# Performance work log

Hardware: AMD Instinct MI355X
Metric: run time of the kernel (lower is better)

Reference implementation:

```python
import jax, jax.numpy as jnp
import numpy as np

NEG_INF = -1e9

def _build_tables():
    # LC0-style 73-plane encoding per from-square: planes 0..55 queen moves
    # (8 directions x 7 distances), 56..63 knight moves. to_sq[from, plane]
    # is the to-square index; valid marks on-board targets.
    to_sq = np.zeros((64, 64), np.int32)
    valid = np.zeros((64, 64), bool)
    dirs = [(1, 0), (1, 1), (0, 1), (-1, 1), (-1, 0), (-1, -1), (0, -1), (1, -1)]
    knights = [(2, 1), (1, 2), (-1, 2), (-2, 1), (-2, -1), (-1, -2), (1, -2), (2, -1)]
    for sq in range(64):
        r, c = divmod(sq, 8)
        for d, (dr, dc) in enumerate(dirs):
            for dist in range(1, 8):
                p = d * 7 + (dist - 1)
                nr, nc = r + dr * dist, c + dc * dist
                if 0 <= nr < 8 and 0 <= nc < 8:
                    to_sq[sq, p] = nr * 8 + nc
                    valid[sq, p] = True
        for i, (dr, dc) in enumerate(knights):
            nr, nc = r + dr, c + dc
            if 0 <= nr < 8 and 0 <= nc < 8:
                to_sq[sq, 56 + i] = nr * 8 + nc
                valid[sq, 56 + i] = True
    promo_from = (np.arange(64) // 8) == 6  # rank 7 pawns (0-indexed rank 6)
    return to_sq, valid, promo_from

TO_SQ_NP, VALID_NP, PROMO_FROM_NP = _build_tables()
TO_SQ = jnp.asarray(TO_SQ_NP)            # (64, 64) int32
TO_VALID = jnp.asarray(VALID_NP)         # (64, 64) bool
PROMO_FROM = jnp.asarray(PROMO_FROM_NP)  # (64,) bool

EMBED_DIM = 1024
POLICY_DIM = 128
SCALE = POLICY_DIM ** (-0.5)


def setup_inputs() -> dict:
    key = jax.random.key(0)
    ks = jax.random.split(key, 4)
    B = 1024
    std = 1.0 / np.sqrt(EMBED_DIM)
    x = jax.random.normal(ks[0], (B, 64, EMBED_DIM), dtype=jnp.float32)
    Wq = jax.random.normal(ks[1], (EMBED_DIM, POLICY_DIM), dtype=jnp.float32) * std
    Wk = jax.random.normal(ks[2], (EMBED_DIM, POLICY_DIM), dtype=jnp.float32) * std
    Wu = jax.random.normal(ks[3], (EMBED_DIM, 9), dtype=jnp.float32) * std
    bq = jnp.zeros((POLICY_DIM,), jnp.float32)
    bk = jnp.zeros((POLICY_DIM,), jnp.float32)
    bu = jnp.zeros((9,), jnp.float32)
    return {"x": x, "Wq": Wq, "bq": bq, "Wk": Wk, "bk": bk, "Wu": Wu, "bu": bu}


def reference(x, Wq, bq, Wk, bk, Wu, bu):
    b = x.shape[0]
    q = jnp.einsum('bsd,dp->bsp', x, Wq) + bq            # (B, 64, P)
    k = jnp.einsum('bsd,dp->bsp', x, Wk) + bk            # (B, 64, P)
    logits_ft = jnp.einsum('bfp,btp->bft', q, k) * SCALE  # (B, 64, 64)
    # gather to-square logits into plane order per from-square
    idx = jnp.broadcast_to(TO_SQ[None].astype(jnp.int32), (b, 64, 64))
    logits_64 = jnp.take_along_axis(logits_ft, idx, axis=-1)  # (B, 64, 64)
    logits_64 = jnp.where(TO_VALID[None], logits_64, jnp.float32(NEG_INF))
    up = jnp.einsum('bsd,dn->bsn', x, Wu) + bu            # (B, 64, 9)
    up = jnp.where(PROMO_FROM[None, :, None], up, jnp.float32(NEG_INF))
    logits = jnp.concatenate([logits_64, up], axis=-1)    # (B, 64, 73)
    return logits.reshape(b, 64 * 73)
```

## Files before the change

### kernel.cpp

```cpp
#include <hip/hip_runtime.h>

#define NEG_INF (-1e9f)
#define SCALE_F 0.08838834764831845f

typedef __attribute__((ext_vector_type(8))) short short8;
typedef __attribute__((ext_vector_type(4))) float float4v;

__device__ __constant__ int cDR[8] = {1,1,0,-1,-1,-1,0,1};
__device__ __constant__ int cDC[8] = {0,1,1,1,0,-1,-1,-1};
__device__ __constant__ int cKR[8] = {2,1,-1,-2,-2,-1,1,2};
__device__ __constant__ int cKC[8] = {1,2,2,1,-1,-2,-2,-1};

__device__ __forceinline__ ushort f2bf(float f) {
  union { float f; unsigned u; } a; a.f = f;
  unsigned u = a.u;
  return (ushort)((u + 0x7FFFu + ((u >> 16) & 1u)) >> 16);
}

__device__ __forceinline__ void glds16(const void* g, void* l) {
  __builtin_amdgcn_global_load_lds(
      (const __attribute__((address_space(1))) unsigned int*)g,
      (__attribute__((address_space(3))) unsigned int*)l, 16, 0, 0);
}

__device__ __forceinline__ short8 pack8(float4 a, float4 b) {
  union { short8 v; unsigned u[4]; } o;
  o.u[0] = (__float_as_uint(a.y) & 0xFFFF0000u) | (__float_as_uint(a.x) >> 16);
  o.u[1] = (__float_as_uint(a.w) & 0xFFFF0000u) | (__float_as_uint(a.z) >> 16);
  o.u[2] = (__float_as_uint(b.y) & 0xFFFF0000u) | (__float_as_uint(b.x) >> 16);
  o.u[3] = (__float_as_uint(b.w) & 0xFFFF0000u) | (__float_as_uint(b.z) >> 16);
  return o.v;
}

__global__ void wconv_kernel(const float* __restrict__ Wq,
                             const float* __restrict__ Wk,
                             const float* __restrict__ Wu,
                             ushort* __restrict__ Wsw) {
  int row = blockIdx.x;
  for (int k = threadIdx.x; k < 1024; k += 256) {
    float v;
    if (row < 128)      v = Wq[k * 128 + row];
    else if (row < 256) v = Wk[k * 128 + (row - 128)];
    else if (row < 265) v = Wu[k * 9 + (row - 256)];
    else                v = 0.f;
    int kc = k >> 5, kin = k & 31, g = kin >> 3, j = kin & 7;
    int sg = g ^ (row & 3);
    Wsw[(size_t)kc * 9216 + row * 32 + sg * 8 + j] = f2bf(v);
  }
}

__global__ __launch_bounds__(256, 2)
void qk_gemm(const float* __restrict__ x,
             const float* __restrict__ bq,
             const float* __restrict__ bk,
             const float* __restrict__ bu,
             const ushort* __restrict__ Wsw,
             ushort* __restrict__ qkbuf,
             float* __restrict__ out) {
  __shared__ __align__(16) char smem[34816];
  char* xsB = smem;
  char* wtB = smem + 16384;

  const int tid = threadIdx.x;
  const int w = tid >> 6, lane = tid & 63;
  const int l15 = lane & 15, qd = lane >> 4;
  const int wm = w >> 1, wn = w & 1;

  const char* xb = (const char*)x + (size_t)blockIdx.x * 524288;
  const char* WsB = (const char*)Wsw + (size_t)lane * 16;

  int xsrc[4];
  #pragma unroll
  for (int c = 0; c < 4; ++c) {
    int s = c * 4 + w;
    int row = s * 8 + (lane >> 3);
    int sg = lane & 7;
    xsrc[c] = row * 4096 + ((sg ^ (row & 7)) * 16);
  }

  float4v acc[4][8];
  #pragma unroll
  for (int i = 0; i < 4; ++i)
    #pragma unroll
    for (int j = 0; j < 8; ++j)
      acc[i][j] = (float4v){0.f, 0.f, 0.f, 0.f};
  float4v aup = (float4v){0.f, 0.f, 0.f, 0.f};

  #pragma unroll 1
  for (int kc = 0; kc < 32; ++kc) {
    #pragma unroll
    for (int c = 0; c < 4; ++c)
      glds16(xb + kc * 128 + xsrc[c], xsB + (c * 4 + w) * 1024);
    const char* wsrc = WsB + (size_t)kc * 18432;
    #pragma unroll
    for (int c = 0; c < 5; ++c) {
      int s = c * 4 + w;
      if (s < 18) glds16(wsrc + s * 1024, wtB + s * 1024);
    }
    __syncthreads();

    short8 af[4];
    #pragma unroll
    for (int mt = 0; mt < 4; ++mt) {
      int row = wm * 64 + mt * 16 + l15;
      int g0 = qd * 2;
      float4 v0 = *(const float4*)(xsB + row * 128 + ((g0 ^ (row & 7)) * 16));
      float4 v1 = *(const float4*)(xsB + row * 128 + (((g0 + 1) ^ (row & 7)) * 16));
      af[mt] = pack8(v0, v1);
    }
    const int gb = (qd ^ (l15 & 3)) * 16;
    short8 bf[8];
    #pragma unroll
    for (int nt = 0; nt < 8; ++nt) {
      int rowB = wn * 128 + nt * 16 + l15;
      bf[nt] = *(const short8*)(wtB + rowB * 64 + gb);
    }
    #pragma unroll
    for (int mt = 0; mt < 4; ++mt)
      #pragma unroll
      for (int nt = 0; nt < 8; ++nt)
        acc[mt][nt] = __builtin_amdgcn_mfma_f32_16x16x32_bf16(
            af[mt], bf[nt], acc[mt][nt], 0, 0, 0);
    if (wn) {
      short8 ub = *(const short8*)(wtB + (256 + l15) * 64 + gb);
      aup = __builtin_amdgcn_mfma_f32_16x16x32_bf16(af[3], ub, aup, 0, 0, 0);
    }
    __syncthreads();
  }

  const int batch = blockIdx.x * 2 + wm;

  if (wn && qd < 2 && l15 < 9) {
    float bias = bu[l15];
    #pragma unroll
    for (int r = 0; r < 4; ++r) {
      int f = 48 + qd * 4 + r;
      out[(size_t)batch * 4672 + f * 73 + 64 + l15] = aup[r] + bias;
    }
  }

  {
    const float* bias_ptr = wn ? bk : bq;
    ushort* dst = qkbuf + (size_t)batch * 16384 + wn * 8192;
    #pragma unroll
    for (int nt = 0; nt < 8; ++nt) {
      int p = nt * 16 + l15;
      float bias = bias_ptr[p];
      int g = p >> 3, j = p & 7;
      #pragma unroll
      for (int mt = 0; mt < 4; ++mt)
        #pragma unroll
        for (int r = 0; r < 4; ++r) {
          int f = mt * 16 + qd * 4 + r;
          float v = acc[mt][nt][r] + bias;
          if (!wn) v *= SCALE_F;
          dst[f * 128 + ((g ^ (f & 7)) * 8) + j] = f2bf(v);
        }
    }
  }
}

__global__ __launch_bounds__(256)
void attn_gather(const ushort* __restrict__ qkbuf,
                 float* __restrict__ out) {
  __shared__ __align__(16) char smem[32768];
  float* Sl = (float*)smem;

  const int tid = threadIdx.x;
  const int w = tid >> 6, lane = tid & 63;
  const int l15 = lane & 15, qd = lane >> 4;

  const char* src = (const char*)qkbuf + (size_t)blockIdx.x * 32768 +
                    (size_t)lane * 16;
  #pragma unroll
  for (int c = 0; c < 8; ++c)
    glds16(src + (c * 4 + w) * 1024, smem + (c * 4 + w) * 1024);
  __syncthreads();

  float4v acc2[4];
  #pragma unroll
  for (int nt = 0; nt < 4; ++nt) acc2[nt] = (float4v){0.f, 0.f, 0.f, 0.f};
  #pragma unroll
  for (int kp = 0; kp < 4; ++kp) {
    int m = w * 16 + l15;
    short8 a2 = *(const short8*)(smem + m * 256 + (((kp * 4 + qd) ^ (m & 7)) * 16));
    #pragma unroll
    for (int nt = 0; nt < 4; ++nt) {
      int t = nt * 16 + l15;
      short8 b2 = *(const short8*)(smem + 16384 + t * 256 +
                                   (((kp * 4 + qd) ^ (t & 7)) * 16));
      acc2[nt] = __builtin_amdgcn_mfma_f32_16x16x32_bf16(a2, b2, acc2[nt], 0, 0, 0);
    }
  }
  __syncthreads();
  #pragma unroll
  for (int nt = 0; nt < 4; ++nt)
    #pragma unroll
    for (int r = 0; r < 4; ++r)
      Sl[(w * 16 + qd * 4 + r) * 65 + nt * 16 + l15] = acc2[nt][r];
  __syncthreads();

  float* outb = out + (size_t)blockIdx.x * 4672;
  for (int idx = tid; idx < 4672; idx += 256) {
    int f = idx / 73;
    int j = idx - f * 73;
    float val;
    if (j < 64) {
      int rr = f >> 3, cc = f & 7;
      int nr, nc;
      if (j < 56) {
        int d = j / 7;
        int dist = j - d * 7 + 1;
        nr = rr + cDR[d] * dist;
        nc = cc + cDC[d] * dist;
      } else {
        nr = rr + cKR[j - 56];
        nc = cc + cKC[j - 56];
      }
      val = (nr >= 0 && nr < 8 && nc >= 0 && nc < 8) ? Sl[f * 65 + nr * 8 + nc]
                                                     : NEG_INF;
    } else {
      if (f >= 48 && f < 56) continue;
      val = NEG_INF;
    }
    outb[idx] = val;
  }
}

extern "C" void kernel_launch(void* const* d_in, const int* in_sizes, int n_in,
                              void* d_out, int out_size, void* d_ws, size_t ws_size,
                              hipStream_t stream) {
  const float* x  = (const float*)d_in[0];
  const float* Wq = (const float*)d_in[1];
  const float* bq = (const float*)d_in[2];
  const float* Wk = (const float*)d_in[3];
  const float* bk = (const float*)d_in[4];
  const float* Wu = (const float*)d_in[5];
  const float* bu = (const float*)d_in[6];
  float* out = (float*)d_out;
  ushort* Wsw   = (ushort*)d_ws;
  ushort* qkbuf = (ushort*)((char*)d_ws + (1 << 20));

  const int B = in_sizes[0] / 65536;

  wconv_kernel<<<288, 256, 0, stream>>>(Wq, Wk, Wu, Wsw);
  qk_gemm<<<B / 2, 256, 0, stream>>>(x, bq, bk, bu, Wsw, qkbuf, out);
  attn_gather<<<B, 256, 0, stream>>>(qkbuf, out);
}
```

Measured before the change: 427.8 us.

## Fuse QK GEMM with attention-gather and double-buffer x tiles

Merges the projection GEMM and the per-board QK^T/gather kernel into one kernel, so Q/K stay in LDS instead of round-tripping through a global bf16 buffer. The x tile load is double-buffered with manual vmcnt waits and raw barriers, so the next chunk's global loads overlap compute. The W slice count drops from 18 to 17 (rows 265+ were zero padding). Address offsets are also precomputed outside the loop. LDS use rises to about 49 KB, which may limit occupancy, and the epilogue serializes the two boards per block.

```diff
diff --git a/kernel.cpp b/kernel.cpp
--- a/kernel.cpp
+++ b/kernel.cpp
@@ -30,6 +30,13 @@
   o.u[2] = (__float_as_uint(b.y) & 0xFFFF0000u) | (__float_as_uint(b.x) >> 16);
   o.u[3] = (__float_as_uint(b.w) & 0xFFFF0000u) | (__float_as_uint(b.z) >> 16);
   return o.v;
+}
+
+__device__ __forceinline__ short8 lds_load8(const ushort* p) {
+  union { short8 v; ushort4 h[2]; } u;
+  u.h[0] = *(const ushort4*)(p);
+  u.h[1] = *(const ushort4*)(p + 4);
+  return u.v;
 }
 
 __global__ void wconv_kernel(const float* __restrict__ Wq,
@@ -50,24 +57,27 @@
 }
 
 __global__ __launch_bounds__(256, 2)
-void qk_gemm(const float* __restrict__ x,
-             const float* __restrict__ bq,
-             const float* __restrict__ bk,
-             const float* __restrict__ bu,
-             const ushort* __restrict__ Wsw,
-             ushort* __restrict__ qkbuf,
-             float* __restrict__ out) {
-  __shared__ __align__(16) char smem[34816];
-  char* xsB = smem;
-  char* wtB = smem + 16384;
+void apol_fused(const float* __restrict__ x,
+                const float* __restrict__ bq,
+                const float* __restrict__ bk,
+                const float* __restrict__ bu,
+                const ushort* __restrict__ Wsw,
+                float* __restrict__ out) {
+  __shared__ __align__(16) char smem[50176];
+  char*   xb0 = smem;
+  char*   xb1 = smem + 16384;
+  char*   wtB = smem + 32768;
+  ushort* qs  = (ushort*)smem;
+  ushort* ks  = (ushort*)(smem + 16896);
+  float*  Sl  = (float*)smem;
 
   const int tid = threadIdx.x;
   const int w = tid >> 6, lane = tid & 63;
   const int l15 = lane & 15, qd = lane >> 4;
   const int wm = w >> 1, wn = w & 1;
 
-  const char* xb = (const char*)x + (size_t)blockIdx.x * 524288;
-  const char* WsB = (const char*)Wsw + (size_t)lane * 16;
+  const char* xg = (const char*)x + (size_t)blockIdx.x * 524288;
+  const char* wg = (const char*)Wsw + (size_t)lane * 16;
 
   int xsrc[4];
   #pragma unroll
@@ -78,6 +88,21 @@
     xsrc[c] = row * 4096 + ((sg ^ (row & 7)) * 16);
   }
 
+  int aoff[4][2];
+  #pragma unroll
+  for (int mt = 0; mt < 4; ++mt) {
+    int row = wm * 64 + mt * 16 + l15;
+    #pragma unroll
+    for (int h = 0; h < 2; ++h)
+      aoff[mt][h] = row * 128 + (((qd * 2 + h) ^ (row & 7)) * 16);
+  }
+  const int gb = (qd ^ (l15 & 3)) * 16;
+  int boff[8];
+  #pragma unroll
+  for (int nt = 0; nt < 8; ++nt)
+    boff[nt] = (wn * 128 + nt * 16 + l15) * 64 + gb;
+  const int uoff = (256 + l15) * 64 + gb;
+
   float4v acc[4][8];
   #pragma unroll
   for (int i = 0; i < 4; ++i)
@@ -86,35 +111,40 @@
       acc[i][j] = (float4v){0.f, 0.f, 0.f, 0.f};
   float4v aup = (float4v){0.f, 0.f, 0.f, 0.f};
 
+  {
+    const char* s0 = wg;
+    #pragma unroll
+    for (int c = 0; c < 5; ++c) {
+      int sg = c * 4 + w;
+      if (sg < 17) glds16(s0 + sg * 1024, wtB + sg * 1024);
+    }
+    #pragma unroll
+    for (int c = 0; c < 4; ++c)
+      glds16(xg + xsrc[c], xb0 + (c * 4 + w) * 1024);
+    #pragma unroll
+    for (int c = 0; c < 4; ++c)
+      glds16(xg + 128 + xsrc[c], xb1 + (c * 4 + w) * 1024);
+  }
+
   #pragma unroll 1
   for (int kc = 0; kc < 32; ++kc) {
-    #pragma unroll
-    for (int c = 0; c < 4; ++c)
-      glds16(xb + kc * 128 + xsrc[c], xsB + (c * 4 + w) * 1024);
-    const char* wsrc = WsB + (size_t)kc * 18432;
-    #pragma unroll
-    for (int c = 0; c < 5; ++c) {
-      int s = c * 4 + w;
-      if (s < 18) glds16(wsrc + s * 1024, wtB + s * 1024);
-    }
-    __syncthreads();
-
+    if (kc == 31) asm volatile("s_waitcnt vmcnt(0)" ::: "memory");
+    else          asm volatile("s_waitcnt vmcnt(4)" ::: "memory");
+    __builtin_amdgcn_s_barrier();
+    asm volatile("" ::: "memory");
+
+    const char* xsB = (kc & 1) ? xb1 : xb0;
     short8 af[4];
     #pragma unroll
     for (int mt = 0; mt < 4; ++mt) {
-      int row = wm * 64 + mt * 16 + l15;
-      int g0 = qd * 2;
-      float4 v0 = *(const float4*)(xsB + row * 128 + ((g0 ^ (row & 7)) * 16));
-      float4 v1 = *(const float4*)(xsB + row * 128 + (((g0 + 1) ^ (row & 7)) * 16));
+      float4 v0 = *(const float4*)(xsB + aoff[mt][0]);
+      float4 v1 = *(const float4*)(xsB + aoff[mt][1]);
       af[mt] = pack8(v0, v1);
     }
-    const int gb = (qd ^ (l15 & 3)) * 16;
     short8 bf[8];
     #pragma unroll
-    for (int nt = 0; nt < 8; ++nt) {
-      int rowB = wn * 128 + nt * 16 + l15;
-      bf[nt] = *(const short8*)(wtB + rowB * 64 + gb);
-    }
+    for (int nt = 0; nt < 8; ++nt)
+      bf[nt] = *(const short8*)(wtB + boff[nt]);
     #pragma unroll
     for (int mt = 0; mt < 4; ++mt)
       #pragma unroll
@@ -122,108 +152,108 @@
         acc[mt][nt] = __builtin_amdgcn_mfma_f32_16x16x32_bf16(
             af[mt], bf[nt], acc[mt][nt], 0, 0, 0);
     if (wn) {
-      short8 ub = *(const short8*)(wtB + (256 + l15) * 64 + gb);
+      short8 ub = *(const short8*)(wtB + uoff);
       aup = __builtin_amdgcn_mfma_f32_16x16x32_bf16(af[3], ub, aup, 0, 0, 0);
     }
-    __syncthreads();
-  }
-
-  const int batch = blockIdx.x * 2 + wm;
+
+    asm volatile("" ::: "memory");
+    __builtin_amdgcn_s_barrier();
+
+    if (kc < 31) {
+      const char* s1 = wg + (size_t)(kc + 1) * 18432;
+      #pragma unroll
+      for (int c = 0; c < 5; ++c) {
+        int sg = c * 4 + w;
+        if (sg < 17) glds16(s1 + sg * 1024, wtB + sg * 1024);
+      }
+    }
+    if (kc < 30) {
+      char* dst = (kc & 1) ? xb1 : xb0;
+      #pragma unroll
+      for (int c = 0; c < 4; ++c)
+        glds16(xg + (kc + 2) * 128 + xsrc[c], dst + (c * 4 + w) * 1024);
+    }
+  }
 
   if (wn && qd < 2 && l15 < 9) {
     float bias = bu[l15];
     #pragma unroll
     for (int r = 0; r < 4; ++r) {
       int f = 48 + qd * 4 + r;
-      out[(size_t)batch * 4672 + f * 73 + 64 + l15] = aup[r] + bias;
-    }
-  }
-
-  {
-    const float* bias_ptr = wn ? bk : bq;
-    ushort* dst = qkbuf + (size_t)batch * 16384 + wn * 8192;
-    #pragma unroll
-    for (int nt = 0; nt < 8; ++nt) {
-      int p = nt * 16 + l15;
-      float bias = bias_ptr[p];
-      int g = p >> 3, j = p & 7;
-      #pragma unroll
-      for (int mt = 0; mt < 4; ++mt)
+      out[(size_t)(blockIdx.x * 2 + wm) * 4672 + f * 73 + 64 + l15] =
+          aup[r] + bias;
+    }
+  }
+
+  #pragma unroll 1
+  for (int bi = 0; bi < 2; ++bi) {
+    __syncthreads();
+    if (wm == bi) {
+      const float* bias_ptr = wn ? bk : bq;
+      ushort* dst = wn ? ks : qs;
+      #pragma unroll
+      for (int nt = 0; nt < 8; ++nt) {
+        int p = nt * 16 + l15;
+        float bias = bias_ptr[p];
         #pragma unroll
-        for (int r = 0; r < 4; ++r) {
-          int f = mt * 16 + qd * 4 + r;
-          float v = acc[mt][nt][r] + bias;
-          if (!wn) v *= SCALE_F;
-          dst[f * 128 + ((g ^ (f & 7)) * 8) + j] = f2bf(v);
+        for (int mt = 0; mt < 4; ++mt)
+          #pragma unroll
+          for (int r = 0; r < 4; ++r) {
+            int row = mt * 16 + qd * 4 + r;
+            float v = acc[mt][nt][r] + bias;
+            if (!wn) v *= SCALE_F;
+            dst[row * 132 + p] = f2bf(v);
+          }
+      }
+    }
+    __syncthreads();
+
+    float4v acc2[4];
+    #pragma unroll
+    for (int nt = 0; nt < 4; ++nt) acc2[nt] = (float4v){0.f, 0.f, 0.f, 0.f};
+    #pragma unroll
+    for (int kp = 0; kp < 4; ++kp) {
+      int kb = kp * 32 + qd * 8;
+      short8 a2 = lds_load8(&qs[(w * 16 + l15) * 132 + kb]);
+      #pragma unroll
+      for (int nt = 0; nt < 4; ++nt) {
+        short8 b2 = lds_load8(&ks[(nt * 16 + l15) * 132 + kb]);
+        acc2[nt] = __builtin_amdgcn_mfma_f32_16x16x32_bf16(a2, b2, acc2[nt], 0, 0, 0);
+      }
+    }
+    __syncthreads();
+    #pragma unroll
+    for (int nt = 0; nt < 4; ++nt)
+      #pragma unroll
+      for (int r = 0; r < 4; ++r)
+        Sl[(w * 16 + qd * 4 + r) * 65 + nt * 16 + l15] = acc2[nt][r];
+    __syncthreads();
+
+    float* outb = out + (size_t)(blockIdx.x * 2 + bi) * 4672;
+    for (int idx = tid; idx < 4672; idx += 256) {
+      int f = idx / 73;
+      int j = idx - f * 73;
+      float val;
+      if (j < 64) {
+        int rr = f >> 3, cc = f & 7;
+        int nr, nc;
+        if (j < 56) {
+          int d = j / 7;
+          int dist = j - d * 7 + 1;
+          nr = rr + cDR[d] * dist;
+          nc = cc + cDC[d] * dist;
+        } else {
+          nr = rr + cKR[j - 56];
+          nc = cc + cKC[j - 56];
         }
-    }
-  }
-}
-
-__global__ __launch_bounds__(256)
-void attn_gather(const ushort* __restrict__ qkbuf,
-                 float* __restrict__ out) {
-  __shared__ __align__(16) char smem[32768];
-  float* Sl = (float*)smem;
-
-  const int tid = threadIdx.x;
-  const int w = tid >> 6, lane = tid & 63;
-  const int l15 = lane & 15, qd = lane >> 4;
-
-  const char* src = (const char*)qkbuf + (size_t)blockIdx.x * 32768 +
-                    (size_t)lane * 16;
-  #pragma unroll
-  for (int c = 0; c < 8; ++c)
-    glds16(src + (c * 4 + w) * 1024, smem + (c * 4 + w) * 1024);
-  __syncthreads();
-
-  float4v acc2[4];
-  #pragma unroll
-  for (int nt = 0; nt < 4; ++nt) acc2[nt] = (float4v){0.f, 0.f, 0.f, 0.f};
-  #pragma unroll
-  for (int kp = 0; kp < 4; ++kp) {
-    int m = w * 16 + l15;
-    short8 a2 = *(const short8*)(smem + m * 256 + (((kp * 4 + qd) ^ (m & 7)) * 16));
-    #pragma unroll
-    for (int nt = 0; nt < 4; ++nt) {
-      int t = nt * 16 + l15;
-      short8 b2 = *(const short8*)(smem + 16384 + t * 256 +
-                                   (((kp * 4 + qd) ^ (t & 7)) * 16));
-      acc2[nt] = __builtin_amdgcn_mfma_f32_16x16x32_bf16(a2, b2, acc2[nt], 0, 0, 0);
-    }
-  }
-  __syncthreads();
-  #pragma unroll
-  for (int nt = 0; nt < 4; ++nt)
-    #pragma unroll
-    for (int r = 0; r < 4; ++r)
-      Sl[(w * 16 + qd * 4 + r) * 65 + nt * 16 + l15] = acc2[nt][r];
-  __syncthreads();
-
-  float* outb = out + (size_t)blockIdx.x * 4672;
-  for (int idx = tid; idx < 4672; idx += 256) {
-    int f = idx / 73;
-    int j = idx - f * 73;
-    float val;
-    if (j < 64) {
-      int rr = f >> 3, cc = f & 7;
-      int nr, nc;
-      if (j < 56) {
-        int d = j / 7;
-        int dist = j - d * 7 + 1;
-        nr = rr + cDR[d] * dist;
-        nc = cc + cDC[d] * dist;
+        val = (nr >= 0 && nr < 8 && nc >= 0 && nc < 8) ? Sl[f * 65 + nr * 8 + nc]
+                                                       : NEG_INF;
       } else {
-        nr = rr + cKR[j - 56];
-        nc = cc + cKC[j - 56];
-      }
-      val = (nr >= 0 && nr < 8 && nc >= 0 && nc < 8) ? Sl[f * 65 + nr * 8 + nc]
-                                                     : NEG_INF;
-    } else {
-      if (f >= 48 && f < 56) continue;
-      val = NEG_INF;
-    }
-    outb[idx] = val;
+        if (f >= 48 && f < 56) continue;
+        val = NEG_INF;
+      }
+      outb[idx] = val;
+    }
   }
 }
 
@@ -238,12 +268,10 @@
   const float* Wu = (const float*)d_in[5];
   const float* bu = (const float*)d_in[6];
   float* out = (float*)d_out;
-  ushort* Wsw   = (ushort*)d_ws;
-  ushort* qkbuf = (ushort*)((char*)d_ws + (1 << 20));
+  ushort* Wsw = (ushort*)d_ws;
 
   const int B = in_sizes[0] / 65536;
 
   wconv_kernel<<<288, 256, 0, stream>>>(Wq, Wk, Wu, Wsw);
-  qk_gemm<<<B / 2, 256, 0, stream>>>(x, bq, bk, bu, Wsw, qkbuf, out);
-  attn_gather<<<B, 256, 0, stream>>>(qkbuf, out);
-}
+  apol_fused<<<B / 2, 256, 0, stream>>>(x, bq, bk, bu, Wsw, out);
+}
```

After: 422.3 us. No clear change (-1.3%).

## Fuse QK projection and attention-gather into one kernel with double-buffered x

Applied to the files above, without the earlier changes.

Merges the projection GEMM and the QK^T/gather kernel into a single per-batch kernel, so Q and K stay in LDS and the bf16 qk round-trip through global memory and the extra launch go away. Weights are pre-laid out in an MFMA-register-friendly order and loaded straight from global (L2) into registers each k-chunk, rather than staged through LDS. x chunks are double-buffered with async global-to-LDS loads and manual waitcnt/barriers so loads overlap the MFMAs. One batch per block, with more blocks per CU, in exchange for heavier per-block weight traffic from L2.

```diff
diff --git a/kernel.cpp b/kernel.cpp
--- a/kernel.cpp
+++ b/kernel.cpp
@@ -35,172 +35,188 @@
 __global__ void wconv_kernel(const float* __restrict__ Wq,
                              const float* __restrict__ Wk,
                              const float* __restrict__ Wu,
-                             ushort* __restrict__ Wsw) {
+                             ushort* __restrict__ Wreg) {
   int row = blockIdx.x;
+  int cb = row >> 4, lr = row & 15;
   for (int k = threadIdx.x; k < 1024; k += 256) {
     float v;
     if (row < 128)      v = Wq[k * 128 + row];
     else if (row < 256) v = Wk[k * 128 + (row - 128)];
     else if (row < 265) v = Wu[k * 9 + (row - 256)];
     else                v = 0.f;
-    int kc = k >> 5, kin = k & 31, g = kin >> 3, j = kin & 7;
-    int sg = g ^ (row & 3);
-    Wsw[(size_t)kc * 9216 + row * 32 + sg * 8 + j] = f2bf(v);
-  }
-}
-
-__global__ __launch_bounds__(256, 2)
-void qk_gemm(const float* __restrict__ x,
-             const float* __restrict__ bq,
-             const float* __restrict__ bk,
-             const float* __restrict__ bu,
-             const ushort* __restrict__ Wsw,
-             ushort* __restrict__ qkbuf,
-             float* __restrict__ out) {
-  __shared__ __align__(16) char smem[34816];
-  char* xsB = smem;
-  char* wtB = smem + 16384;
+    int kc = k >> 5, kin = k & 31, qd = kin >> 3, j = kin & 7;
+    Wreg[kc * 8704 + cb * 512 + qd * 128 + lr * 8 + j] = f2bf(v);
+  }
+}
+
+__global__ __launch_bounds__(256, 4)
+void apol_fused(const float* __restrict__ x,
+                const float* __restrict__ bq,
+                const float* __restrict__ bk,
+                const float* __restrict__ bu,
+                const ushort* Wreg,
+                float* __restrict__ out) {
+  __shared__ __align__(16) char xb0[8192];
+  __shared__ __align__(16) char xb1[8192];
+  __shared__ __align__(16) char kbuf[16384];
 
   const int tid = threadIdx.x;
   const int w = tid >> 6, lane = tid & 63;
   const int l15 = lane & 15, qd = lane >> 4;
-  const int wm = w >> 1, wn = w & 1;
-
-  const char* xb = (const char*)x + (size_t)blockIdx.x * 524288;
-  const char* WsB = (const char*)Wsw + (size_t)lane * 16;
-
-  int xsrc[4];
-  #pragma unroll
-  for (int c = 0; c < 4; ++c) {
-    int s = c * 4 + w;
+
+  const char* xg = (const char*)x + (size_t)blockIdx.x * 262144;
+  const char* wgl = (const char*)Wreg + (size_t)lane * 16;
+
+  int xsrc[2], xdst[2];
+  #pragma unroll
+  for (int c = 0; c < 2; ++c) {
+    int s = w * 2 + c;
     int row = s * 8 + (lane >> 3);
-    int sg = lane & 7;
-    xsrc[c] = row * 4096 + ((sg ^ (row & 7)) * 16);
-  }
-
-  float4v acc[4][8];
+    xsrc[c] = row * 4096 + (((lane & 7) ^ (row & 7)) * 16);
+    xdst[c] = s * 1024;
+  }
+
+  float4v acc[4][4];
   #pragma unroll
   for (int i = 0; i < 4; ++i)
     #pragma unroll
-    for (int j = 0; j < 8; ++j)
+    for (int j = 0; j < 4; ++j)
       acc[i][j] = (float4v){0.f, 0.f, 0.f, 0.f};
   float4v aup = (float4v){0.f, 0.f, 0.f, 0.f};
 
+  short8 bf[4], ub;
+
+  glds16(xg + 0 * 128 + xsrc[0], xb0 + xdst[0]);
+  glds16(xg + 0 * 128 + xsrc[1], xb0 + xdst[1]);
+  glds16(xg + 1 * 128 + xsrc[0], xb1 + xdst[0]);
+  glds16(xg + 1 * 128 + xsrc[1], xb1 + xdst[1]);
+  asm volatile("" ::: "memory");
+  {
+    const char* wp = wgl;
+    #pragma unroll
+    for (int nt = 0; nt < 4; ++nt)
+      bf[nt] = *(const short8*)(wp + (w * 4 + nt) * 1024);
+    ub = *(const short8*)(wp + 16 * 1024);
+  }
+  asm volatile("" ::: "memory");
+
+#define KBODY(KC, XBUF)                                                        \
+  do {                                                                         \
+    if ((KC) == 31) __builtin_amdgcn_s_waitcnt(0xF75);           \
+    else            __builtin_amdgcn_s_waitcnt(0xF77);           \
+    __builtin_amdgcn_s_barrier();                                              \
+    asm volatile("" ::: "memory");                                             \
+    short8 af[4];                                                              \
+    _Pragma("unroll") for (int mt = 0; mt < 4; ++mt) {                         \
+      int row = mt * 16 + l15;                                                 \
+      float4 v0 = *(const float4*)(XBUF + row * 128 +                          \
+                                   (((qd * 2) ^ (row & 7)) * 16));             \
+      float4 v1 = *(const float4*)(XBUF + row * 128 +                          \
+                                   (((qd * 2 + 1) ^ (row & 7)) * 16));         \
+      af[mt] = pack8(v0, v1);                                                  \
+    }                                                                          \
+    _Pragma("unroll") for (int mt = 0; mt < 4; ++mt)                           \
+      _Pragma("unroll") for (int nt = 0; nt < 4; ++nt)                         \
+          acc[mt][nt] = __builtin_amdgcn_mfma_f32_16x16x32_bf16(               \
+              af[mt], bf[nt], acc[mt][nt], 0, 0, 0);                           \
+    aup = __builtin_amdgcn_mfma_f32_16x16x32_bf16(af[3], ub, aup, 0, 0, 0);    \
+    asm volatile("" ::: "memory");                                             \
+    __builtin_amdgcn_s_barrier();                                              \
+    if ((KC) < 31) {    \
+      const char* wp = wgl + (size_t)((KC) + 1) * 17408;                       \
+      _Pragma("unroll") for (int nt = 0; nt < 4; ++nt)                         \
+          bf[nt] = *(const short8*)(wp + (w * 4 + nt) * 1024);                 \
+      ub = *(const short8*)(wp + 16 * 1024);                                   \
+    }                                                                          \
+    asm volatile("" ::: "memory");                                             \
+    if ((KC) < 30) {  \
+      glds16(xg + ((KC) + 2) * 128 + xsrc[0], XBUF + xdst[0]);                 \
+      glds16(xg + ((KC) + 2) * 128 + xsrc[1], XBUF + xdst[1]);                 \
+    }                                                                          \
+    asm volatile("" ::: "memory");                                             \
+  } while (0)
+
   #pragma unroll 1
-  for (int kc = 0; kc < 32; ++kc) {
-    #pragma unroll
-    for (int c = 0; c < 4; ++c)
-      glds16(xb + kc * 128 + xsrc[c], xsB + (c * 4 + w) * 1024);
-    const char* wsrc = WsB + (size_t)kc * 18432;
-    #pragma unroll
-    for (int c = 0; c < 5; ++c) {
-      int s = c * 4 + w;
-      if (s < 18) glds16(wsrc + s * 1024, wtB + s * 1024);
-    }
-    __syncthreads();
-
-    short8 af[4];
-    #pragma unroll
-    for (int mt = 0; mt < 4; ++mt) {
-      int row = wm * 64 + mt * 16 + l15;
-      int g0 = qd * 2;
-      float4 v0 = *(const float4*)(xsB + row * 128 + ((g0 ^ (row & 7)) * 16));
-      float4 v1 = *(const float4*)(xsB + row * 128 + (((g0 + 1) ^ (row & 7)) * 16));
-      af[mt] = pack8(v0, v1);
-    }
-    const int gb = (qd ^ (l15 & 3)) * 16;
-    short8 bf[8];
-    #pragma unroll
-    for (int nt = 0; nt < 8; ++nt) {
-      int rowB = wn * 128 + nt * 16 + l15;
-      bf[nt] = *(const short8*)(wtB + rowB * 64 + gb);
-    }
-    #pragma unroll
-    for (int mt = 0; mt < 4; ++mt)
-      #pragma unroll
-      for (int nt = 0; nt < 8; ++nt)
-        acc[mt][nt] = __builtin_amdgcn_mfma_f32_16x16x32_bf16(
-            af[mt], bf[nt], acc[mt][nt], 0, 0, 0);
-    if (wn) {
-      short8 ub = *(const short8*)(wtB + (256 + l15) * 64 + gb);
-      aup = __builtin_amdgcn_mfma_f32_16x16x32_bf16(af[3], ub, aup, 0, 0, 0);
-    }
-    __syncthreads();
-  }
-
-  const int batch = blockIdx.x * 2 + wm;
-
-  if (wn && qd < 2 && l15 < 9) {
+  for (int kc2 = 0; kc2 < 16; ++kc2) {
+    KBODY(kc2 * 2, xb0);
+    KBODY(kc2 * 2 + 1, xb1);
+  }
+#undef KBODY
+
+  float* outb = out + (size_t)blockIdx.x * 4672;
+
+  if (w == 3 && qd < 2 && l15 < 9) {
     float bias = bu[l15];
     #pragma unroll
-    for (int r = 0; r < 4; ++r) {
-      int f = 48 + qd * 4 + r;
-      out[(size_t)batch * 4672 + f * 73 + 64 + l15] = aup[r] + bias;
-    }
-  }
+    for (int r = 0; r < 4; ++r)
+      outb[(48 + qd * 4 + r) * 73 + 64 + l15] = aup[r] + bias;
+  }
+
+  __syncthreads();
 
   {
-    const float* bias_ptr = wn ? bk : bq;
-    ushort* dst = qkbuf + (size_t)batch * 16384 + wn * 8192;
-    #pragma unroll
-    for (int nt = 0; nt < 8; ++nt) {
-      int p = nt * 16 + l15;
+    const bool isq = (w < 2);
+    const float* bias_ptr = isq ? bq : bk;
+    #pragma unroll
+    for (int nt = 0; nt < 4; ++nt) {
+      int p = (w & 1) * 64 + nt * 16 + l15;
       float bias = bias_ptr[p];
-      int g = p >> 3, j = p & 7;
+      int pg = p >> 3, pj = p & 7;
       #pragma unroll
       for (int mt = 0; mt < 4; ++mt)
         #pragma unroll
         for (int r = 0; r < 4; ++r) {
-          int f = mt * 16 + qd * 4 + r;
+          int row = mt * 16 + qd * 4 + r;
           float v = acc[mt][nt][r] + bias;
-          if (!wn) v *= SCALE_F;
-          dst[f * 128 + ((g ^ (f & 7)) * 8) + j] = f2bf(v);
+          ushort* dst;
+          int lrow;
+          if (isq) {
+            v *= SCALE_F;
+            dst = (ushort*)((row & 32) ? xb1 : xb0);
+            lrow = row & 31;
+          } else {
+            dst = (ushort*)kbuf;
+            lrow = row;
+          }
+          dst[lrow * 128 + ((pg ^ (row & 7)) * 8) + pj] = f2bf(v);
         }
     }
   }
-}
-
-__global__ __launch_bounds__(256)
-void attn_gather(const ushort* __restrict__ qkbuf,
-                 float* __restrict__ out) {
-  __shared__ __align__(16) char smem[32768];
-  float* Sl = (float*)smem;
-
-  const int tid = threadIdx.x;
-  const int w = tid >> 6, lane = tid & 63;
-  const int l15 = lane & 15, qd = lane >> 4;
-
-  const char* src = (const char*)qkbuf + (size_t)blockIdx.x * 32768 +
-                    (size_t)lane * 16;
-  #pragma unroll
-  for (int c = 0; c < 8; ++c)
-    glds16(src + (c * 4 + w) * 1024, smem + (c * 4 + w) * 1024);
   __syncthreads();
 
   float4v acc2[4];
   #pragma unroll
   for (int nt = 0; nt < 4; ++nt) acc2[nt] = (float4v){0.f, 0.f, 0.f, 0.f};
-  #pragma unroll
-  for (int kp = 0; kp < 4; ++kp) {
-    int m = w * 16 + l15;
-    short8 a2 = *(const short8*)(smem + m * 256 + (((kp * 4 + qd) ^ (m & 7)) * 16));
-    #pragma unroll
-    for (int nt = 0; nt < 4; ++nt) {
-      int t = nt * 16 + l15;
-      short8 b2 = *(const short8*)(smem + 16384 + t * 256 +
-                                   (((kp * 4 + qd) ^ (t & 7)) * 16));
-      acc2[nt] = __builtin_amdgcn_mfma_f32_16x16x32_bf16(a2, b2, acc2[nt], 0, 0, 0);
-    }
-  }
-  __syncthreads();
+  {
+    const ushort* qb = (const ushort*)((w & 2) ? xb1 : xb0);
+    const ushort* kb = (const ushort*)kbuf;
+    int mrow = w * 16 + l15;
+    #pragma unroll
+    for (int kp = 0; kp < 4; ++kp) {
+      int g = kp * 4 + qd;
+      short8 a2 = *(const short8*)(qb + (mrow & 31) * 128 +
+                                   ((g ^ (mrow & 7)) * 8));
+      #pragma unroll
+      for (int nt = 0; nt < 4; ++nt) {
+        int t = nt * 16 + l15;
+        short8 b2 = *(const short8*)(kb + t * 128 + ((g ^ (t & 7)) * 8));
+        acc2[nt] = __builtin_amdgcn_mfma_f32_16x16x32_bf16(a2, b2, acc2[nt], 0, 0, 0);
+      }
+    }
+  }
+  __syncthreads();
+
+  float* Slf = (float*)kbuf;
   #pragma unroll
   for (int nt = 0; nt < 4; ++nt)
     #pragma unroll
-    for (int r = 0; r < 4; ++r)
-      Sl[(w * 16 + qd * 4 + r) * 65 + nt * 16 + l15] = acc2[nt][r];
-  __syncthreads();
-
-  float* outb = out + (size_t)blockIdx.x * 4672;
+    for (int r = 0; r < 4; ++r) {
+      int row = w * 16 + qd * 4 + r;
+      int col = nt * 16 + l15;
+      Slf[row * 64 + (((col >> 3) ^ (row & 7)) * 8) + (col & 7)] = acc2[nt][r];
+    }
+  __syncthreads();
+
   for (int idx = tid; idx < 4672; idx += 256) {
     int f = idx / 73;
     int j = idx - f * 73;
@@ -217,8 +233,12 @@
         nr = rr + cKR[j - 56];
         nc = cc + cKC[j - 56];
       }
-      val = (nr >= 0 && nr < 8 && nc >= 0 && nc < 8) ? Sl[f * 65 + nr * 8 + nc]
-                                                     : NEG_INF;
+      if (nr >= 0 && nr < 8 && nc >= 0 && nc < 8) {
+        int t = nr * 8 + nc;
+        val = Slf[f * 64 + (((t >> 3) ^ (f & 7)) * 8) + (t & 7)];
+      } else {
+        val = NEG_INF;
+      }
     } else {
       if (f >= 48 && f < 56) continue;
       val = NEG_INF;
@@ -238,12 +258,10 @@
   const float* Wu = (const float*)d_in[5];
   const float* bu = (const float*)d_in[6];
   float* out = (float*)d_out;
-  ushort* Wsw   = (ushort*)d_ws;
-  ushort* qkbuf = (ushort*)((char*)d_ws + (1 << 20));
+  ushort* Wreg = (ushort*)d_ws;
 
   const int B = in_sizes[0] / 65536;
 
-  wconv_kernel<<<288, 256, 0, stream>>>(Wq, Wk, Wu, Wsw);
-  qk_gemm<<<B / 2, 256, 0, stream>>>(x, bq, bk, bu, Wsw, qkbuf, out);
-  attn_gather<<<B, 256, 0, stream>>>(qkbuf, out);
-}
+  wconv_kernel<<<272, 256, 0, stream>>>(Wq, Wk, Wu, Wreg);
+  apol_fused<<<B, 256, 0, stream>>>(x, bq, bk, bu, Wreg, out);
+}
```

Measured after the change: 416.5 us. -2.7%, faster.
